# Performance work log

Hardware: AMD Instinct MI355X
Metric: run time of the kernel (lower is better)

Reference implementation:

```python
import jax, jax.numpy as jnp
import numpy as np

KS = 3
ST = 1


def _windows(x, ks, st):
    """im2col sliding windows: (bs, c, h, w) -> (bs, c, H', W', ks, ks)
    where windows[b,c,i,j,k,f] = x[b,c, i*st+k, j*st+f] (matches torch as_strided)."""
    bs, c, h, w = x.shape
    Hp = (h - ks) // st + 1
    Wp = (w - ks) // st + 1
    return jnp.stack(
        [jnp.stack([x[:, :, k:k + Hp * st:st, f:f + Wp * st:st] for f in range(ks)], axis=-1)
         for k in range(ks)], axis=-2)


def setup_inputs() -> dict:
    key = jax.random.key(0)
    k1, k2, k3 = jax.random.split(key, 3)
    x = jax.random.normal(k1, (16, 16, 64, 512), dtype=jnp.float32)
    points = jax.random.normal(k2, (16, 3, 64, 512), dtype=jnp.float32)
    kernel = jax.random.normal(k3, (32, 16, 4), dtype=jnp.float32) * 0.05
    return {"x": x, "kernel": kernel, "points": points}


def reference(x, kernel, points):
    ks, st = KS, ST
    # (bs, in_c, H', W', ks, ks) overlapping patches of features and xyz coords
    strided_x = _windows(x, ks, st)
    strided_pts = _windows(points, ks, st)
    bd = ks // 2 if st == 1 else ks // 4
    # center point of each window: (bs, 3, H', W')
    ctr = points[:, :, bd:-bd, bd:-bd][:, :, ::st, ::st]
    # point-relative coordinates per window element: (bs, 3, H', W', ks, ks)
    rel_pts = ctr[..., None, None] - strided_pts
    # homogeneous coordinate -> d = 4
    rel_pts = jnp.concatenate([rel_pts, jnp.ones_like(rel_pts[:, :1])], axis=1)
    # kernel: (out_c, in_c, 4)
    return jnp.einsum('bdhwkf,bihwkf,oid->bohw', rel_pts, strided_x, kernel)
```

## Files before the change

kernel.cpp:

```cpp
#include <hip/hip_runtime.h>
#include <hip/hip_bf16.h>


#define HH 64
#define WW 512
#define HP 62
#define WP 510
#define IC 16
#define OC 32
#define BS 16
#define RB 2

typedef __attribute__((ext_vector_type(8))) short short8;
typedef __attribute__((ext_vector_type(4))) float f32x4;

struct __attribute__((packed, aligned(4))) F4U { float x, y, z, w; };

static __device__ __forceinline__ short f2bf(float f) {
    union { __hip_bfloat16 h; short s; } u;
    u.h = __float2bfloat16(f);
    return u.s;
}

template<bool EDGE>
static __device__ __forceinline__ void run_wave(
    const float* __restrict__ x, const float* __restrict__ kern,
    const float* __restrict__ pts, float* __restrict__ out,
    int b, int i0, int j0, int p, int c)
{
    const int j = j0 + p;
    const int jl = EDGE ? (j > WW - 4 ? WW - 4 : j) : j;
    const bool sh = EDGE && (j > WW - 4);

    short8 a0lo, a0hi, a1lo, a1hi;
    {
        const float4* k0v = (const float4*)(kern + (size_t)p * 64 + c * 8);
        const float4* k1v = (const float4*)(kern + (size_t)(16 + p) * 64 + c * 8);
        float4 v0a = k0v[0], v0b = k0v[1], v0c = k0v[8], v0d = k0v[9];
        float4 v1a = k1v[0], v1b = k1v[1], v1c = k1v[8], v1d = k1v[9];
        a0lo[0]=f2bf(v0a.x); a0lo[1]=f2bf(v0a.y); a0lo[2]=f2bf(v0a.z); a0lo[3]=f2bf(v0a.w);
        a0lo[4]=f2bf(v0b.x); a0lo[5]=f2bf(v0b.y); a0lo[6]=f2bf(v0b.z); a0lo[7]=f2bf(v0b.w);
        a0hi[0]=f2bf(v0c.x); a0hi[1]=f2bf(v0c.y); a0hi[2]=f2bf(v0c.z); a0hi[3]=f2bf(v0c.w);
        a0hi[4]=f2bf(v0d.x); a0hi[5]=f2bf(v0d.y); a0hi[6]=f2bf(v0d.z); a0hi[7]=f2bf(v0d.w);
        a1lo[0]=f2bf(v1a.x); a1lo[1]=f2bf(v1a.y); a1lo[2]=f2bf(v1a.z); a1lo[3]=f2bf(v1a.w);
        a1lo[4]=f2bf(v1b.x); a1lo[5]=f2bf(v1b.y); a1lo[6]=f2bf(v1b.z); a1lo[7]=f2bf(v1b.w);
        a1hi[0]=f2bf(v1c.x); a1hi[1]=f2bf(v1c.y); a1hi[2]=f2bf(v1c.z); a1hi[3]=f2bf(v1c.w);
        a1hi[4]=f2bf(v1d.x); a1hi[5]=f2bf(v1d.y); a1hi[6]=f2bf(v1d.z); a1hi[7]=f2bf(v1d.w);
    }

    float xs[4][RB], px0[4][RB], px1[4][RB], px2[4][RB];
    #pragma unroll
    for (int t = 0; t < 4; ++t)
        #pragma unroll
        for (int q = 0; q < RB; ++q) { xs[t][q]=0.f; px0[t][q]=0.f; px1[t][q]=0.f; px2[t][q]=0.f; }
    float c0[RB], c1[RB], c2[RB];

    const float* pbase = pts + (size_t)b * 3 * HH * WW;
    const float* xbase = x + (size_t)b * IC * HH * WW;

    #pragma unroll
    for (int rr = 0; rr < RB + 2; ++rr) {
        const size_t roff = (size_t)(i0 + rr) * WW + jl;
        F4U pv0 = *(const F4U*)(pbase + roff);
        F4U pv1 = *(const F4U*)(pbase + (size_t)HH * WW + roff);
        F4U pv2 = *(const F4U*)(pbase + 2 * (size_t)HH * WW + roff);
        const float pa0 = sh ? pv0.y : pv0.x, pm0 = sh ? pv0.z : pv0.y, pz0 = sh ? pv0.w : pv0.z;
        const float pa1 = sh ? pv1.y : pv1.x, pm1 = sh ? pv1.z : pv1.y, pz1 = sh ? pv1.w : pv1.z;
        const float pa2 = sh ? pv2.y : pv2.x, pm2 = sh ? pv2.z : pv2.y, pz2 = sh ? pv2.w : pv2.z;
        if (rr >= 1 && rr <= RB) { c0[rr-1] = pm0; c1[rr-1] = pm1; c2[rr-1] = pm2; }
        #pragma unroll
        for (int t = 0; t < 4; ++t) {
            const int ic = (t >> 1) * 8 + 2 * c + (t & 1);
            F4U xv = *(const F4U*)(xbase + (size_t)ic * HH * WW + roff);
            const float xa = sh ? xv.y : xv.x, xm = sh ? xv.z : xv.y, xz = sh ? xv.w : xv.z;
            const float rsx = xa + xm + xz;
            float r0 = pa0 * xa; r0 = fmaf(pm0, xm, r0); r0 = fmaf(pz0, xz, r0);
            float r1 = pa1 * xa; r1 = fmaf(pm1, xm, r1); r1 = fmaf(pz1, xz, r1);
            float r2 = pa2 * xa; r2 = fmaf(pm2, xm, r2); r2 = fmaf(pz2, xz, r2);
            #pragma unroll
            for (int q = 0; q < RB; ++q) {
                if (rr >= q && rr <= q + 2) {
                    xs[t][q] += rsx; px0[t][q] += r0; px1[t][q] += r1; px2[t][q] += r2;
                }
            }
        }
    }

    #pragma unroll
    for (int q = 0; q < RB; ++q) {
        short8 blo, bhi;
        #pragma unroll
        for (int t = 0; t < 4; ++t) {
            const short t0 = f2bf(fmaf(c0[q], xs[t][q], -px0[t][q]));
            const short t1 = f2bf(fmaf(c1[q], xs[t][q], -px1[t][q]));
            const short t2 = f2bf(fmaf(c2[q], xs[t][q], -px2[t][q]));
            const short t3 = f2bf(xs[t][q]);
            const int s = (t & 1) * 4;
            if (t < 2) { blo[s+0]=t0; blo[s+1]=t1; blo[s+2]=t2; blo[s+3]=t3; }
            else       { bhi[s+0]=t0; bhi[s+1]=t1; bhi[s+2]=t2; bhi[s+3]=t3; }
        }
        f32x4 acc0 = {0.f,0.f,0.f,0.f}, acc1 = {0.f,0.f,0.f,0.f};
        acc0 = __builtin_amdgcn_mfma_f32_16x16x32_bf16(a0lo, blo, acc0, 0, 0, 0);
        acc0 = __builtin_amdgcn_mfma_f32_16x16x32_bf16(a0hi, bhi, acc0, 0, 0, 0);
        acc1 = __builtin_amdgcn_mfma_f32_16x16x32_bf16(a1lo, blo, acc1, 0, 0, 0);
        acc1 = __builtin_amdgcn_mfma_f32_16x16x32_bf16(a1hi, bhi, acc1, 0, 0, 0);
        if (j < WP) {
            float* ob = out + (size_t)b * OC * HP * WP + (size_t)(i0 + q) * WP + j;
            #pragma unroll
            for (int r = 0; r < 4; ++r) {
                const int o = c * 4 + r;
                ob[(size_t)o * HP * WP]        = acc0[r];
                ob[(size_t)(o + 16) * HP * WP] = acc1[r];
            }
        }
    }
}

__global__ __launch_bounds__(256) void flex_conv_mfma2(
    const float* __restrict__ x, const float* __restrict__ kern,
    const float* __restrict__ pts, float* __restrict__ out)
{
    const int lane = threadIdx.x & 63;
    const int wave = threadIdx.x >> 6;
    const int strip = blockIdx.x * 4 + wave;
    const int j0 = strip * 16;
    const int i0 = blockIdx.y * RB;
    const int b  = blockIdx.z;
    const int p = lane & 15;
    const int c = lane >> 4;
    if (j0 + 15 <= WW - 4) run_wave<false>(x, kern, pts, out, b, i0, j0, p, c);
    else                   run_wave<true >(x, kern, pts, out, b, i0, j0, p, c);
}

extern "C" void kernel_launch(void* const* d_in, const int* in_sizes, int n_in,
                              void* d_out, int out_size, void* d_ws, size_t ws_size,
                              hipStream_t stream)
{
    const float* x    = (const float*)d_in[0];
    const float* kern = (const float*)d_in[1];
    const float* pts  = (const float*)d_in[2];
    float* out = (float*)d_out;

    dim3 block(256, 1, 1);
    dim3 grid(8, HP / RB, BS);
    flex_conv_mfma2<<<grid, block, 0, stream>>>(x, kern, pts, out);
}
```

Baseline: 122.5 us.

## Stage input tiles in LDS and raise output rows per block

The kernel now loads a 64-column by (RB+2)-row tile of all 16 feature planes and 3 point planes into shared memory with aligned float4 loads. Waves then read their 3-wide windows from LDS instead of issuing unaligned global loads. RB goes from 2 to 4, so the overlapping halo rows are re-fetched less often. The last row block is clamped to overlap its neighbour, and the cost is a block-wide barrier plus about 31KB of LDS per block, which may reduce occupancy.

```diff
diff --git a/kernel.cpp b/kernel.cpp
--- a/kernel.cpp
+++ b/kernel.cpp
@@ -9,12 +9,17 @@
 #define IC 16
 #define OC 32
 #define BS 16
-#define RB 2
+#define RB 4
+#define TR (RB + 2)
+#define TC 64
+#define LC 68
+#define NPL 19
+#define CPR 17
+#define NROWS (NPL * TR)
+#define NCHUNK (NROWS * CPR)
 
 typedef __attribute__((ext_vector_type(8))) short short8;
 typedef __attribute__((ext_vector_type(4))) float f32x4;
-
-struct __attribute__((packed, aligned(4))) F4U { float x, y, z, w; };
 
 static __device__ __forceinline__ short f2bf(float f) {
     union { __hip_bfloat16 h; short s; } u;
@@ -22,15 +27,45 @@
     return u.s;
 }
 
-template<bool EDGE>
-static __device__ __forceinline__ void run_wave(
+__global__ __launch_bounds__(256) void flex_conv_lds(
     const float* __restrict__ x, const float* __restrict__ kern,
-    const float* __restrict__ pts, float* __restrict__ out,
-    int b, int i0, int j0, int p, int c)
+    const float* __restrict__ pts, float* __restrict__ out)
 {
-    const int j = j0 + p;
-    const int jl = EDGE ? (j > WW - 4 ? WW - 4 : j) : j;
-    const bool sh = EDGE && (j > WW - 4);
+    __shared__ float lds[NPL * TR * LC];
+
+    const int tid = threadIdx.x;
+    const int j0 = blockIdx.x * TC;
+    int i0 = blockIdx.y * RB;
+    if (i0 > HP - RB) i0 = HP - RB;
+    const int b = blockIdx.z;
+
+    const float* xb = x + (size_t)b * IC * HH * WW;
+    const float* pb = pts + (size_t)b * 3 * HH * WW;
+
+    #pragma unroll
+    for (int rnd = 0; rnd < 8; ++rnd) {
+        const int cid = tid + rnd * 256;
+        if (cid < NCHUNK) {
+            const int row = cid / CPR;
+            const int chunk = cid - row * CPR;
+            const int plane = row / TR;
+            const int rr = row - plane * TR;
+            const float* base = (plane < IC)
+                ? (xb + (size_t)plane * HH * WW)
+                : (pb + (size_t)(plane - IC) * HH * WW);
+            int gcol = j0 + chunk * 4;
+            if (gcol > WW - 4) gcol = WW - 4;
+            const float4 v = *(const float4*)(base + (size_t)(i0 + rr) * WW + gcol);
+            *(float4*)(&lds[row * LC + chunk * 4]) = v;
+        }
+    }
+    __syncthreads();
+
+    const int lane = tid & 63;
+    const int wave = tid >> 6;
+    const int p = lane & 15;
+    const int c = lane >> 4;
+    const int tc = wave * 16 + p;
 
     short8 a0lo, a0hi, a1lo, a1hi;
     {
@@ -55,28 +90,24 @@
         for (int q = 0; q < RB; ++q) { xs[t][q]=0.f; px0[t][q]=0.f; px1[t][q]=0.f; px2[t][q]=0.f; }
     float c0[RB], c1[RB], c2[RB];
 
-    const float* pbase = pts + (size_t)b * 3 * HH * WW;
-    const float* xbase = x + (size_t)b * IC * HH * WW;
-
     #pragma unroll
-    for (int rr = 0; rr < RB + 2; ++rr) {
-        const size_t roff = (size_t)(i0 + rr) * WW + jl;
-        F4U pv0 = *(const F4U*)(pbase + roff);
-        F4U pv1 = *(const F4U*)(pbase + (size_t)HH * WW + roff);
-        F4U pv2 = *(const F4U*)(pbase + 2 * (size_t)HH * WW + roff);
-        const float pa0 = sh ? pv0.y : pv0.x, pm0 = sh ? pv0.z : pv0.y, pz0 = sh ? pv0.w : pv0.z;
-        const float pa1 = sh ? pv1.y : pv1.x, pm1 = sh ? pv1.z : pv1.y, pz1 = sh ? pv1.w : pv1.z;
-        const float pa2 = sh ? pv2.y : pv2.x, pm2 = sh ? pv2.z : pv2.y, pz2 = sh ? pv2.w : pv2.z;
+    for (int rr = 0; rr < TR; ++rr) {
+        const float* lp0 = &lds[(IC * TR + rr) * LC + tc];
+        const float* lp1 = &lds[((IC + 1) * TR + rr) * LC + tc];
+        const float* lp2 = &lds[((IC + 2) * TR + rr) * LC + tc];
+        const float pa0 = lp0[0], pm0 = lp0[1], pz0 = lp0[2];
+        const float pa1 = lp1[0], pm1 = lp1[1], pz1 = lp1[2];
+        const float pa2 = lp2[0], pm2 = lp2[1], pz2 = lp2[2];
         if (rr >= 1 && rr <= RB) { c0[rr-1] = pm0; c1[rr-1] = pm1; c2[rr-1] = pm2; }
         #pragma unroll
         for (int t = 0; t < 4; ++t) {
             const int ic = (t >> 1) * 8 + 2 * c + (t & 1);
-            F4U xv = *(const F4U*)(xbase + (size_t)ic * HH * WW + roff);
-            const float xa = sh ? xv.y : xv.x, xm = sh ? xv.z : xv.y, xz = sh ? xv.w : xv.z;
-            const float rsx = xa + xm + xz;
-            float r0 = pa0 * xa; r0 = fmaf(pm0, xm, r0); r0 = fmaf(pz0, xz, r0);
-            float r1 = pa1 * xa; r1 = fmaf(pm1, xm, r1); r1 = fmaf(pz1, xz, r1);
-            float r2 = pa2 * xa; r2 = fmaf(pm2, xm, r2); r2 = fmaf(pz2, xz, r2);
+            const float* lx = &lds[(ic * TR + rr) * LC + tc];
+            const float x0 = lx[0], x1 = lx[1], x2 = lx[2];
+            const float rsx = x0 + x1 + x2;
+            float r0 = pa0 * x0; r0 = fmaf(pm0, x1, r0); r0 = fmaf(pz0, x2, r0);
+            float r1 = pa1 * x0; r1 = fmaf(pm1, x1, r1); r1 = fmaf(pz1, x2, r1);
+            float r2 = pa2 * x0; r2 = fmaf(pm2, x1, r2); r2 = fmaf(pz2, x2, r2);
             #pragma unroll
             for (int q = 0; q < RB; ++q) {
                 if (rr >= q && rr <= q + 2) {
@@ -86,6 +117,7 @@
         }
     }
 
+    const int j = j0 + tc;
     #pragma unroll
     for (int q = 0; q < RB; ++q) {
         short8 blo, bhi;
@@ -116,22 +148,6 @@
     }
 }
 
-__global__ __launch_bounds__(256) void flex_conv_mfma2(
-    const float* __restrict__ x, const float* __restrict__ kern,
-    const float* __restrict__ pts, float* __restrict__ out)
-{
-    const int lane = threadIdx.x & 63;
-    const int wave = threadIdx.x >> 6;
-    const int strip = blockIdx.x * 4 + wave;
-    const int j0 = strip * 16;
-    const int i0 = blockIdx.y * RB;
-    const int b  = blockIdx.z;
-    const int p = lane & 15;
-    const int c = lane >> 4;
-    if (j0 + 15 <= WW - 4) run_wave<false>(x, kern, pts, out, b, i0, j0, p, c);
-    else                   run_wave<true >(x, kern, pts, out, b, i0, j0, p, c);
-}
-
 extern "C" void kernel_launch(void* const* d_in, const int* in_sizes, int n_in,
                               void* d_out, int out_size, void* d_ws, size_t ws_size,
                               hipStream_t stream)
@@ -142,6 +158,6 @@
     float* out = (float*)d_out;
 
     dim3 block(256, 1, 1);
-    dim3 grid(8, HP / RB, BS);
-    flex_conv_mfma2<<<grid, block, 0, stream>>>(x, kern, pts, out);
+    dim3 grid(WW / TC, (HP + RB - 1) / RB, BS);
+    flex_conv_lds<<<grid, block, 0, stream>>>(x, kern, pts, out);
 }
```

Result: faster. 113.7 us (-7.2%).

## March each wave down eight output rows with a rolling three-row reduction ring

Applied to the files above, without the earlier changes.

Each wave now computes 8 consecutive output rows instead of 2, keeping per-row partial reductions in a three-entry register ring so every input row is loaded and reduced once rather than up to three times. Next-row loads are issued before the current row's MFMA, giving software prefetch. The last row block is clamped to overlap (i0 = HP-8), so some rows are recomputed and written twice. The grid shrinks to 8 row blocks, with higher register pressure and fewer total waves.

```diff
diff --git a/kernel.cpp b/kernel.cpp
--- a/kernel.cpp
+++ b/kernel.cpp
@@ -9,11 +9,11 @@
 #define IC 16
 #define OC 32
 #define BS 16
-#define RB 2
+#define MR 8
+#define YS 8
 
 typedef __attribute__((ext_vector_type(8))) short short8;
 typedef __attribute__((ext_vector_type(4))) float f32x4;
-
 struct __attribute__((packed, aligned(4))) F4U { float x, y, z, w; };
 
 static __device__ __forceinline__ short f2bf(float f) {
@@ -22,15 +22,62 @@
     return u.s;
 }
 
+struct RowRed {
+    float rsx[4], r0[4], r1[4], r2[4];
+    float pm0, pm1, pm2;
+};
+
 template<bool EDGE>
-static __device__ __forceinline__ void run_wave(
+static __device__ __forceinline__ RowRed reduceRow(const F4U xv[4], const F4U pv[3], bool sh)
+{
+    RowRed rr;
+    const float a0 = (EDGE && sh) ? pv[0].y : pv[0].x;
+    const float m0 = (EDGE && sh) ? pv[0].z : pv[0].y;
+    const float z0 = (EDGE && sh) ? pv[0].w : pv[0].z;
+    const float a1 = (EDGE && sh) ? pv[1].y : pv[1].x;
+    const float m1 = (EDGE && sh) ? pv[1].z : pv[1].y;
+    const float z1 = (EDGE && sh) ? pv[1].w : pv[1].z;
+    const float a2 = (EDGE && sh) ? pv[2].y : pv[2].x;
+    const float m2 = (EDGE && sh) ? pv[2].z : pv[2].y;
+    const float z2 = (EDGE && sh) ? pv[2].w : pv[2].z;
+    rr.pm0 = m0; rr.pm1 = m1; rr.pm2 = m2;
+    #pragma unroll
+    for (int t = 0; t < 4; ++t) {
+        const float xa = (EDGE && sh) ? xv[t].y : xv[t].x;
+        const float xm = (EDGE && sh) ? xv[t].z : xv[t].y;
+        const float xz = (EDGE && sh) ? xv[t].w : xv[t].z;
+        rr.rsx[t] = xa + xm + xz;
+        float v0 = a0 * xa; v0 = fmaf(m0, xm, v0); v0 = fmaf(z0, xz, v0);
+        float v1 = a1 * xa; v1 = fmaf(m1, xm, v1); v1 = fmaf(z1, xz, v1);
+        float v2 = a2 * xa; v2 = fmaf(m2, xm, v2); v2 = fmaf(z2, xz, v2);
+        rr.r0[t] = v0; rr.r1[t] = v1; rr.r2[t] = v2;
+    }
+    return rr;
+}
+
+template<bool EDGE>
+static __device__ __forceinline__ void march(
     const float* __restrict__ x, const float* __restrict__ kern,
     const float* __restrict__ pts, float* __restrict__ out,
-    int b, int i0, int j0, int p, int c)
-{
+    int b, int i0, int j0, int lane)
+{
+    const int p = lane & 15;
+    const int c = lane >> 4;
     const int j = j0 + p;
-    const int jl = EDGE ? (j > WW - 4 ? WW - 4 : j) : j;
+    const int jl = (EDGE && j > WW - 4) ? (WW - 4) : j;
     const bool sh = EDGE && (j > WW - 4);
+
+    const float* xb = x + (size_t)b * IC * HH * WW;
+    const float* pb = pts + (size_t)b * 3 * HH * WW;
+
+    unsigned xoff[4], poff[3];
+    #pragma unroll
+    for (int t = 0; t < 4; ++t) {
+        const int ic = (t >> 1) * 8 + 2 * c + (t & 1);
+        xoff[t] = (unsigned)(ic * HH * WW + jl);
+    }
+    #pragma unroll
+    for (int d = 0; d < 3; ++d) poff[d] = (unsigned)(d * HH * WW + jl);
 
     short8 a0lo, a0hi, a1lo, a1hi;
     {
@@ -48,64 +95,66 @@
         a1hi[4]=f2bf(v1d.x); a1hi[5]=f2bf(v1d.y); a1hi[6]=f2bf(v1d.z); a1hi[7]=f2bf(v1d.w);
     }
 
-    float xs[4][RB], px0[4][RB], px1[4][RB], px2[4][RB];
-    #pragma unroll
-    for (int t = 0; t < 4; ++t)
-        #pragma unroll
-        for (int q = 0; q < RB; ++q) { xs[t][q]=0.f; px0[t][q]=0.f; px1[t][q]=0.f; px2[t][q]=0.f; }
-    float c0[RB], c1[RB], c2[RB];
-
-    const float* pbase = pts + (size_t)b * 3 * HH * WW;
-    const float* xbase = x + (size_t)b * IC * HH * WW;
-
-    #pragma unroll
-    for (int rr = 0; rr < RB + 2; ++rr) {
-        const size_t roff = (size_t)(i0 + rr) * WW + jl;
-        F4U pv0 = *(const F4U*)(pbase + roff);
-        F4U pv1 = *(const F4U*)(pbase + (size_t)HH * WW + roff);
-        F4U pv2 = *(const F4U*)(pbase + 2 * (size_t)HH * WW + roff);
-        const float pa0 = sh ? pv0.y : pv0.x, pm0 = sh ? pv0.z : pv0.y, pz0 = sh ? pv0.w : pv0.z;
-        const float pa1 = sh ? pv1.y : pv1.x, pm1 = sh ? pv1.z : pv1.y, pz1 = sh ? pv1.w : pv1.z;
-        const float pa2 = sh ? pv2.y : pv2.x, pm2 = sh ? pv2.z : pv2.y, pz2 = sh ? pv2.w : pv2.z;
-        if (rr >= 1 && rr <= RB) { c0[rr-1] = pm0; c1[rr-1] = pm1; c2[rr-1] = pm2; }
+    F4U x0v[4], p0v[3], x1v[4], p1v[3], x2v[4], p2v[3];
+    {
+        const unsigned r0o = (unsigned)(i0 * WW);
+        const unsigned r1o = r0o + WW;
+        const unsigned r2o = r1o + WW;
         #pragma unroll
         for (int t = 0; t < 4; ++t) {
-            const int ic = (t >> 1) * 8 + 2 * c + (t & 1);
-            F4U xv = *(const F4U*)(xbase + (size_t)ic * HH * WW + roff);
-            const float xa = sh ? xv.y : xv.x, xm = sh ? xv.z : xv.y, xz = sh ? xv.w : xv.z;
-            const float rsx = xa + xm + xz;
-            float r0 = pa0 * xa; r0 = fmaf(pm0, xm, r0); r0 = fmaf(pz0, xz, r0);
-            float r1 = pa1 * xa; r1 = fmaf(pm1, xm, r1); r1 = fmaf(pz1, xz, r1);
-            float r2 = pa2 * xa; r2 = fmaf(pm2, xm, r2); r2 = fmaf(pz2, xz, r2);
+            x0v[t] = *(const F4U*)(xb + xoff[t] + r0o);
+            x1v[t] = *(const F4U*)(xb + xoff[t] + r1o);
+            x2v[t] = *(const F4U*)(xb + xoff[t] + r2o);
+        }
+        #pragma unroll
+        for (int d = 0; d < 3; ++d) {
+            p0v[d] = *(const F4U*)(pb + poff[d] + r0o);
+            p1v[d] = *(const F4U*)(pb + poff[d] + r1o);
+            p2v[d] = *(const F4U*)(pb + poff[d] + r2o);
+        }
+    }
+    RowRed ring0 = reduceRow<EDGE>(x0v, p0v, sh);
+    RowRed ring1 = reduceRow<EDGE>(x1v, p1v, sh);
+    RowRed ring2 = reduceRow<EDGE>(x2v, p2v, sh);
+
+    float* ob0 = out + (size_t)b * OC * HP * WP + (size_t)i0 * WP + j;
+
+    #pragma unroll
+    for (int s = 0; s < MR; ++s) {
+        F4U nx[4], np[3];
+        if (s < MR - 1) {
+            const unsigned ro = (unsigned)((i0 + s + 3) * WW);
             #pragma unroll
-            for (int q = 0; q < RB; ++q) {
-                if (rr >= q && rr <= q + 2) {
-                    xs[t][q] += rsx; px0[t][q] += r0; px1[t][q] += r1; px2[t][q] += r2;
-                }
-            }
-        }
-    }
-
-    #pragma unroll
-    for (int q = 0; q < RB; ++q) {
+            for (int t = 0; t < 4; ++t) nx[t] = *(const F4U*)(xb + xoff[t] + ro);
+            #pragma unroll
+            for (int d = 0; d < 3; ++d) np[d] = *(const F4U*)(pb + poff[d] + ro);
+        }
+
+        const float c0 = ring1.pm0, c1 = ring1.pm1, c2 = ring1.pm2;
         short8 blo, bhi;
         #pragma unroll
         for (int t = 0; t < 4; ++t) {
-            const short t0 = f2bf(fmaf(c0[q], xs[t][q], -px0[t][q]));
-            const short t1 = f2bf(fmaf(c1[q], xs[t][q], -px1[t][q]));
-            const short t2 = f2bf(fmaf(c2[q], xs[t][q], -px2[t][q]));
-            const short t3 = f2bf(xs[t][q]);
-            const int s = (t & 1) * 4;
-            if (t < 2) { blo[s+0]=t0; blo[s+1]=t1; blo[s+2]=t2; blo[s+3]=t3; }
-            else       { bhi[s+0]=t0; bhi[s+1]=t1; bhi[s+2]=t2; bhi[s+3]=t3; }
-        }
+            const float xs = ring0.rsx[t] + ring1.rsx[t] + ring2.rsx[t];
+            const float q0 = ring0.r0[t] + ring1.r0[t] + ring2.r0[t];
+            const float q1 = ring0.r1[t] + ring1.r1[t] + ring2.r1[t];
+            const float q2 = ring0.r2[t] + ring1.r2[t] + ring2.r2[t];
+            const short e0 = f2bf(fmaf(c0, xs, -q0));
+            const short e1 = f2bf(fmaf(c1, xs, -q1));
+            const short e2 = f2bf(fmaf(c2, xs, -q2));
+            const short e3 = f2bf(xs);
+            const int sl = (t & 1) * 4;
+            if (t < 2) { blo[sl+0]=e0; blo[sl+1]=e1; blo[sl+2]=e2; blo[sl+3]=e3; }
+            else       { bhi[sl+0]=e0; bhi[sl+1]=e1; bhi[sl+2]=e2; bhi[sl+3]=e3; }
+        }
+
         f32x4 acc0 = {0.f,0.f,0.f,0.f}, acc1 = {0.f,0.f,0.f,0.f};
         acc0 = __builtin_amdgcn_mfma_f32_16x16x32_bf16(a0lo, blo, acc0, 0, 0, 0);
         acc0 = __builtin_amdgcn_mfma_f32_16x16x32_bf16(a0hi, bhi, acc0, 0, 0, 0);
         acc1 = __builtin_amdgcn_mfma_f32_16x16x32_bf16(a1lo, blo, acc1, 0, 0, 0);
         acc1 = __builtin_amdgcn_mfma_f32_16x16x32_bf16(a1hi, bhi, acc1, 0, 0, 0);
+
         if (j < WP) {
-            float* ob = out + (size_t)b * OC * HP * WP + (size_t)(i0 + q) * WP + j;
+            float* ob = ob0 + (size_t)s * WP;
             #pragma unroll
             for (int r = 0; r < 4; ++r) {
                 const int o = c * 4 + r;
@@ -113,23 +162,28 @@
                 ob[(size_t)(o + 16) * HP * WP] = acc1[r];
             }
         }
-    }
-}
-
-__global__ __launch_bounds__(256) void flex_conv_mfma2(
+
+        ring0 = ring1;
+        ring1 = ring2;
+        if (s < MR - 1) ring2 = reduceRow<EDGE>(nx, np, sh);
+    }
+}
+
+__global__ __launch_bounds__(256, 3) void flex_conv_march(
     const float* __restrict__ x, const float* __restrict__ kern,
     const float* __restrict__ pts, float* __restrict__ out)
 {
-    const int lane = threadIdx.x & 63;
-    const int wave = threadIdx.x >> 6;
+    const int tid = threadIdx.x;
+    const int lane = tid & 63;
+    const int wave = tid >> 6;
     const int strip = blockIdx.x * 4 + wave;
     const int j0 = strip * 16;
-    const int i0 = blockIdx.y * RB;
-    const int b  = blockIdx.z;
-    const int p = lane & 15;
-    const int c = lane >> 4;
-    if (j0 + 15 <= WW - 4) run_wave<false>(x, kern, pts, out, b, i0, j0, p, c);
-    else                   run_wave<true >(x, kern, pts, out, b, i0, j0, p, c);
+    int i0 = blockIdx.y * MR;
+    if (i0 > HP - MR) i0 = HP - MR;
+    const int b = blockIdx.z;
+
+    if (strip == 31) march<true >(x, kern, pts, out, b, i0, j0, lane);
+    else             march<false>(x, kern, pts, out, b, i0, j0, lane);
 }
 
 extern "C" void kernel_launch(void* const* d_in, const int* in_sizes, int n_in,
@@ -142,6 +196,6 @@
     float* out = (float*)d_out;
 
     dim3 block(256, 1, 1);
-    dim3 grid(8, HP / RB, BS);
-    flex_conv_mfma2<<<grid, block, 0, stream>>>(x, kern, pts, out);
-}
+    dim3 grid(8, YS, BS);
+    flex_conv_march<<<grid, block, 0, stream>>>(x, kern, pts, out);
+}
```

New measurement: 125.6 us. 2.5% more time.
